# Performance work log

Hardware: AMD Instinct MI355X
Metric: run time of the kernel (lower is better)

The kernel has to match this reference:

```python
import jax, jax.numpy as jnp
import numpy as np

N, L, D = 4, 4096, 1024
H = 16
HD = D // H          # 64
MLP = 4 * D          # 4096
EPS = 1e-5

def log_g(x):
    # torch: where(x>=0, log(relu(x)+0.5), -softplus(-x))
    return jnp.where(x >= 0.0, jnp.log(jax.nn.relu(x) + 0.5), -jax.nn.softplus(-x))

def parallel_scan_log(log_coeffs, log_values):
    # log_coeffs: (B, L, C); log_values: (B, L+1, C)
    a_star = jnp.pad(jnp.cumsum(log_coeffs, axis=1), ((0, 0), (1, 0), (0, 0)))
    log_h = jax.lax.cumlogsumexp(log_values - a_star, axis=1)
    return jnp.exp(a_star[:, 1:] + log_h[:, 1:])

def layer_norm(x, gamma, beta):
    mu = jnp.mean(x, axis=-1, keepdims=True)
    var = jnp.var(x, axis=-1, keepdims=True)
    return (x - mu) * jax.lax.rsqrt(var + EPS) * gamma + beta

def setup_inputs() -> dict:
    key = jax.random.key(0)
    ks = jax.random.split(key, 12)
    s = 0.02
    return {
        "x": jax.random.normal(ks[0], (N, L, D), jnp.float32),
        "h_0": jax.random.normal(ks[1], (N, 1, D), jnp.float32),
        "w_in": jax.random.normal(ks[2], (D, D), jnp.float32) * s,
        "b_in": jnp.zeros((D,), jnp.float32),
        "wz": jax.random.normal(ks[3], (HD, HD), jnp.float32) * s,
        "bz": jnp.zeros((HD,), jnp.float32),
        "wh": jax.random.normal(ks[4], (HD, HD), jnp.float32) * s,
        "bh": jnp.zeros((HD,), jnp.float32),
        "w_out": jax.random.normal(ks[5], (D, D), jnp.float32) * s,
        "b_out": jnp.zeros((D,), jnp.float32),
        "ln1_g": jnp.ones((D,), jnp.float32),
        "ln1_b": jnp.zeros((D,), jnp.float32),
        "ln2_g": jnp.ones((D,), jnp.float32),
        "ln2_b": jnp.zeros((D,), jnp.float32),
        "mw1": jax.random.normal(ks[6], (D, MLP), jnp.float32) * s,
        "mb1": jnp.zeros((MLP,), jnp.float32),
        "mw2": jax.random.normal(ks[7], (MLP, MLP), jnp.float32) * s,
        "mb2": jnp.zeros((MLP,), jnp.float32),
        "mw3": jax.random.normal(ks[8], (MLP, D), jnp.float32) * s,
        "mb3": jnp.zeros((D,), jnp.float32),
    }

def reference(x, h_0, w_in, b_in, wz, bz, wh, bh, w_out, b_out,
              ln1_g, ln1_b, ln2_g, ln2_b, mw1, mb1, mw2, mb2, mw3, mb3):
    n, l, d = x.shape
    rnn_input = layer_norm(x, ln1_g, ln1_b)
    pi = rnn_input @ w_in + b_in                                 # (N,L,D)
    pi = pi.reshape(n, l, H, HD).transpose(0, 2, 1, 3).reshape(n * H, l, HD)
    h0 = h_0.reshape(n, 1, H, HD).transpose(0, 2, 1, 3).reshape(n * H, 1, HD)
    # minGRU in log-space
    k = pi @ wz + bz
    log_z = -jax.nn.softplus(-k)
    log_coeffs = -jax.nn.softplus(k)
    log_h0 = log_g(h0)
    log_th = log_g(pi @ wh + bh)
    h = parallel_scan_log(log_coeffs, jnp.concatenate([log_h0, log_z + log_th], axis=1))
    rnn_states = h.reshape(n, H, l, HD).transpose(0, 2, 1, 3).reshape(n, l, d)
    x = x + (rnn_states @ w_out + b_out)
    mlp_in = layer_norm(x, ln2_g, ln2_b)
    y = jax.nn.silu(mlp_in @ mw1 + mb1)
    y = jax.nn.silu(y @ mw2 + mb2)
    y = y @ mw3 + mb3
    return (x + y, rnn_states)
```

## Files before the change

kernel.cpp:

```cpp
#include <hip/hip_runtime.h>
#include <hip/hip_bf16.h>

typedef __attribute__((ext_vector_type(8))) short short8;
typedef __attribute__((ext_vector_type(4))) float f32x4;
using bf16 = __hip_bfloat16;

#define DEV static __device__ __forceinline__

DEV float bf2f(bf16 v) { return __bfloat162float(v); }
DEV bf16 f2bf(float v) { return __float2bfloat16(v); }

DEV void gld_lds16(const void* g, void* l) {
  __builtin_amdgcn_global_load_lds(
      (const __attribute__((address_space(1))) void*)g,
      (__attribute__((address_space(3))) void*)l, 16, 0, 0);
}

__global__ __launch_bounds__(256)
void wconv_kernel(const float* __restrict__ w, bf16* __restrict__ wT, int K, int N) {
  __shared__ float tile[32][33];
  const int kt = blockIdx.x * 32, nt = blockIdx.y * 32;
  const int tx = threadIdx.x & 31, ty = threadIdx.x >> 5;
#pragma unroll
  for (int i = 0; i < 32; i += 8)
    tile[ty + i][tx] = w[(size_t)(kt + ty + i) * N + nt + tx];
  __syncthreads();
#pragma unroll
  for (int i = 0; i < 32; i += 8)
    wT[(size_t)(nt + ty + i) * K + kt + tx] = f2bf(tile[tx][ty + i]);
}

__global__ __launch_bounds__(256)
void ln_kernel(const float* __restrict__ x, const float* __restrict__ g,
               const float* __restrict__ b, bf16* __restrict__ out) {
  const int row = blockIdx.x;
  const int t = threadIdx.x;
  const float4 v = ((const float4*)(x + (size_t)row * 1024))[t];
  float s = v.x + v.y + v.z + v.w;
  float ss = v.x * v.x + v.y * v.y + v.z * v.z + v.w * v.w;
#pragma unroll
  for (int off = 32; off > 0; off >>= 1) {
    s += __shfl_down(s, off);
    ss += __shfl_down(ss, off);
  }
  __shared__ float red[8];
  if ((t & 63) == 0) { red[(t >> 6) * 2] = s; red[(t >> 6) * 2 + 1] = ss; }
  __syncthreads();
  s = red[0] + red[2] + red[4] + red[6];
  ss = red[1] + red[3] + red[5] + red[7];
  const float mu = s * (1.f / 1024.f);
  const float rstd = rsqrtf(ss * (1.f / 1024.f) - mu * mu + 1e-5f);
  const float4 g4 = ((const float4*)g)[t];
  const float4 b4 = ((const float4*)b)[t];
  struct alignas(8) B4 { bf16 v[4]; } o;
  o.v[0] = f2bf((v.x - mu) * rstd * g4.x + b4.x);
  o.v[1] = f2bf((v.y - mu) * rstd * g4.y + b4.y);
  o.v[2] = f2bf((v.z - mu) * rstd * g4.z + b4.z);
  o.v[3] = f2bf((v.w - mu) * rstd * g4.w + b4.w);
  *(B4*)(out + (size_t)row * 1024 + t * 4) = o;
}

template <int EPI>
__global__ __launch_bounds__(256, 2)
void gemm128(const bf16* __restrict__ A, const bf16* __restrict__ BT,
             const float* __restrict__ bias, const float* __restrict__ res,
             void* __restrict__ C, int M, int N, int K) {
  __shared__ short As[128 * 64];
  __shared__ short Bs[128 * 64];
  const int tid = threadIdx.x;
  const int l = tid & 63;
  const int w = tid >> 6;
  const int wr = w >> 1, wc = w & 1;

  const int nbn = N >> 7;
  const int nwg = gridDim.x;
  const int bid = blockIdx.x;
  const int q = nwg >> 3, r = nwg & 7;
  const int xcd = bid & 7, lin = bid >> 3;
  const int wg = (xcd < r ? xcd * (q + 1) : r * (q + 1) + (xcd - r) * q) + lin;
  const int bm = wg / nbn, bn = wg % nbn;

  const bf16* Ab = A + (size_t)bm * 128 * K;
  const bf16* Bb = BT + (size_t)bn * 128 * K;

  f32x4 acc[4][4];
#pragma unroll
  for (int i = 0; i < 4; ++i)
#pragma unroll
    for (int j = 0; j < 4; ++j) acc[i][j] = (f32x4){0.f, 0.f, 0.f, 0.f};

  const int srow = l >> 3;
  const int scol = (((l & 7) ^ (l >> 3)) << 3);

  for (int k0 = 0; k0 < K; k0 += 64) {
    __syncthreads();
#pragma unroll
    for (int p = 0; p < 4; ++p) {
      const int rowA = p * 32 + w * 8 + srow;
      gld_lds16(Ab + (size_t)rowA * K + k0 + scol, As + (p * 32 + w * 8) * 64);
      gld_lds16(Bb + (size_t)rowA * K + k0 + scol, Bs + (p * 32 + w * 8) * 64);
    }
    __syncthreads();
    const int xr = (l & 7) << 3;
#pragma unroll
    for (int kk = 0; kk < 2; ++kk) {
      short8 fa[4], fb[4];
#pragma unroll
      for (int m = 0; m < 4; ++m)
        fa[m] = *(const short8*)&As[(wr * 64 + m * 16 + (l & 15)) * 64 +
                                    ((kk * 32 + (l >> 4) * 8) ^ xr)];
#pragma unroll
      for (int n = 0; n < 4; ++n)
        fb[n] = *(const short8*)&Bs[(wc * 64 + n * 16 + (l & 15)) * 64 +
                                    ((kk * 32 + (l >> 4) * 8) ^ xr)];
#pragma unroll
      for (int m = 0; m < 4; ++m)
#pragma unroll
        for (int n = 0; n < 4; ++n)
          acc[m][n] = __builtin_amdgcn_mfma_f32_16x16x32_bf16(fa[m], fb[n], acc[m][n], 0, 0, 0);
    }
  }

  const int lc = l & 15;
  const int lr = (l >> 4) * 4;
#pragma unroll
  for (int n = 0; n < 4; ++n) {
    const int col = bn * 128 + wc * 64 + n * 16 + lc;
    const float bv = bias[col];
#pragma unroll
    for (int m = 0; m < 4; ++m) {
      const int row = bm * 128 + wr * 64 + m * 16 + lr;
#pragma unroll
      for (int r2 = 0; r2 < 4; ++r2) {
        float v = acc[m][n][r2] + bv;
        const size_t off = (size_t)(row + r2) * N + col;
        if constexpr (EPI == 1) v = v / (1.f + __expf(-v));
        if constexpr (EPI == 2) {
          ((float*)C)[off] = res[off] + v;
        } else {
          ((bf16*)C)[off] = f2bf(v);
        }
      }
    }
  }
  (void)M;
}

template <int EPI>
__global__ __launch_bounds__(512, 2)
void gemm256(const bf16* __restrict__ A, const bf16* __restrict__ BT,
             const float* __restrict__ bias, const float* __restrict__ res,
             void* __restrict__ C, int M, int N, int K) {
  __shared__ alignas(16) short As[2][256 * 64];
  __shared__ alignas(16) short Bs[2][256 * 64];
  const int tid = threadIdx.x;
  const int l = tid & 63;
  const int w = tid >> 6;
  const int wr = w >> 2;
  const int wc = w & 3;

  const int nbn = N >> 8;
  const int nwg = gridDim.x;
  const int bid = blockIdx.x;
  const int q = nwg >> 3, r = nwg & 7;
  const int xcd = bid & 7, lin = bid >> 3;
  const int wg = (xcd < r ? xcd * (q + 1) : r * (q + 1) + (xcd - r) * q) + lin;
  const int bm = wg / nbn, bn = wg % nbn;

  const bf16* Ab = A + (size_t)bm * 256 * K;
  const bf16* Bb = BT + (size_t)bn * 256 * K;

  const int gcol = ((l & 7) ^ (l >> 3)) << 3;
  const int fr = l & 15;
  const int kq = (l >> 4) << 3;
  const int xr = (l & 7) << 3;

  f32x4 acc[8][4];
#pragma unroll
  for (int i = 0; i < 8; ++i)
#pragma unroll
    for (int j = 0; j < 4; ++j) acc[i][j] = (f32x4){0.f, 0.f, 0.f, 0.f};

  short8 fa[2][2], fb[4][2];

#define STAGE_A(BUF, HALF, KT)                                                     \
  do {                                                                             \
    const int rl_ = (HALF) * 128 + w * 16;                                         \
    gld_lds16(Ab + (size_t)(rl_ + (l >> 3)) * K + (KT) * 64 + gcol,                \
              &As[BUF][rl_ * 64]);                                                 \
    gld_lds16(Ab + (size_t)(rl_ + 8 + (l >> 3)) * K + (KT) * 64 + gcol,            \
              &As[BUF][(rl_ + 8) * 64]);                                           \
  } while (0)

#define STAGE_B(BUF, HALF, KT)                                                     \
  do {                                                                             \
    const int rl_ = (HALF) * 128 + w * 16;                                         \
    gld_lds16(Bb + (size_t)(rl_ + (l >> 3)) * K + (KT) * 64 + gcol,                \
              &Bs[BUF][rl_ * 64]);                                                 \
    gld_lds16(Bb + (size_t)(rl_ + 8 + (l >> 3)) * K + (KT) * 64 + gcol,            \
              &Bs[BUF][(rl_ + 8) * 64]);                                           \
  } while (0)

#define LDA2(BUF, M0)                                                                          \
  do {                                                                                         \
    fa[0][0] = *(const short8*)&As[BUF][(wr * 128 + (M0) * 16 + fr) * 64 + (kq ^ xr)];         \
    fa[0][1] = *(const short8*)&As[BUF][(wr * 128 + (M0) * 16 + fr) * 64 + ((32 + kq) ^ xr)];  \
    fa[1][0] = *(const short8*)&As[BUF][(wr * 128 + (M0)*16 + 16 + fr) * 64 + (kq ^ xr)];      \
    fa[1][1] = *(const short8*)&As[BUF][(wr * 128 + (M0)*16 + 16 + fr) * 64 + ((32 + kq) ^ xr)]; \
  } while (0)

#define LDB8(BUF)                                                                              \
  do {                                                                                         \
    _Pragma("unroll") for (int n_ = 0; n_ < 4; ++n_) {                                         \
      fb[n_][0] = *(const short8*)&Bs[BUF][(wc * 64 + n_ * 16 + fr) * 64 + (kq ^ xr)];         \
      fb[n_][1] = *(const short8*)&Bs[BUF][(wc * 64 + n_ * 16 + fr) * 64 + ((32 + kq) ^ xr)];  \
    }                                                                                          \
  } while (0)

#define MMA_PAIR(M0)                                                                           \
  do {                                                                                         \
    _Pragma("unroll") for (int n_ = 0; n_ < 4; ++n_) {                                         \
      acc[M0][n_] = __builtin_amdgcn_mfma_f32_16x16x32_bf16(fa[0][0], fb[n_][0], acc[M0][n_], 0, 0, 0); \
      acc[(M0) + 1][n_] = __builtin_amdgcn_mfma_f32_16x16x32_bf16(fa[1][0], fb[n_][0], acc[(M0) + 1][n_], 0, 0, 0); \
      acc[M0][n_] = __builtin_amdgcn_mfma_f32_16x16x32_bf16(fa[0][1], fb[n_][1], acc[M0][n_], 0, 0, 0); \
      acc[(M0) + 1][n_] = __builtin_amdgcn_mfma_f32_16x16x32_bf16(fa[1][1], fb[n_][1], acc[(M0) + 1][n_], 0, 0, 0); \
    }                                                                                          \
  } while (0)

#define PHASE(CBUF, M0, ...)                                                       \
  do {                                                                             \
    LDA2(CBUF, M0);                                                                \
    __VA_ARGS__;                                                                   \
    __builtin_amdgcn_s_barrier();                                                  \
    asm volatile("s_waitcnt lgkmcnt(0)");                                          \
    __builtin_amdgcn_s_setprio(1);                                                 \
    MMA_PAIR(M0);                                                                  \
    __builtin_amdgcn_s_setprio(0);                                                 \
    __builtin_amdgcn_s_barrier();                                                  \
  } while (0)

#define PHASE_END(CBUF, ...)                                                       \
  do {                                                                             \
    LDA2(CBUF, 6);                                                                 \
    __VA_ARGS__;                                                                   \
    __builtin_amdgcn_s_barrier();                                                  \
    asm volatile("s_waitcnt lgkmcnt(0)");                                          \
    __builtin_amdgcn_s_setprio(1);                                                 \
    MMA_PAIR(6);                                                                   \
    __builtin_amdgcn_s_setprio(0);                                                 \
    if (more) asm volatile("s_waitcnt vmcnt(4)" ::: "memory");                     \
    else      asm volatile("s_waitcnt vmcnt(0)" ::: "memory");                     \
    __builtin_amdgcn_s_barrier();                                                  \
  } while (0)

  STAGE_A(0, 0, 0); STAGE_A(0, 1, 0);
  STAGE_B(0, 0, 0); STAGE_B(0, 1, 0);
  STAGE_B(1, 0, 1); STAGE_B(1, 1, 1);
  asm volatile("s_waitcnt vmcnt(4)" ::: "memory");
  __builtin_amdgcn_s_barrier();

  const int NT = K >> 6;
  const int NI = NT >> 1;
#pragma unroll 1
  for (int i = 0; i < NI; ++i) {
    const int t0 = i * 2;
    const bool more = (i + 1) < NI;
    LDB8(0);
    PHASE(0, 0, STAGE_A(1, 0, t0 + 1));
    PHASE(0, 2, STAGE_A(1, 1, t0 + 1));
    PHASE(0, 4, if (more) STAGE_B(0, 0, t0 + 2));
    PHASE_END(0, if (more) STAGE_B(0, 1, t0 + 2));
    LDB8(1);
    PHASE(1, 0, if (more) STAGE_A(0, 0, t0 + 2));
    PHASE(1, 2, if (more) STAGE_A(0, 1, t0 + 2));
    PHASE(1, 4, if (more) STAGE_B(1, 0, t0 + 3));
    PHASE_END(1, if (more) STAGE_B(1, 1, t0 + 3));
  }

#undef STAGE_A
#undef STAGE_B
#undef LDA2
#undef LDB8
#undef MMA_PAIR
#undef PHASE
#undef PHASE_END

  const int lc = l & 15;
  const int lr = (l >> 4) * 4;
#pragma unroll
  for (int n = 0; n < 4; ++n) {
    const int col = bn * 256 + wc * 64 + n * 16 + lc;
    const float bv = bias[col];
#pragma unroll
    for (int m = 0; m < 8; ++m) {
      const int row = bm * 256 + wr * 128 + m * 16 + lr;
#pragma unroll
      for (int r2 = 0; r2 < 4; ++r2) {
        float v = acc[m][n][r2] + bv;
        const size_t off = (size_t)(row + r2) * N + col;
        if constexpr (EPI == 1) v = v / (1.f + __expf(-v));
        if constexpr (EPI == 2) {
          ((float*)C)[off] = res[off] + v;
        } else {
          ((bf16*)C)[off] = f2bf(v);
        }
      }
    }
  }
  (void)M;
}

__global__ __launch_bounds__(256)
void heads_kernel(const bf16* __restrict__ piB,
                  const float* __restrict__ wz, const float* __restrict__ bz,
                  const float* __restrict__ wh, const float* __restrict__ bh,
                  bf16* __restrict__ aB, bf16* __restrict__ bB) {
  __shared__ float wzs[4096], whs[4096], pis[4096];
  const int h = blockIdx.y;
  const int t0 = blockIdx.x * 64;
  const int tid = threadIdx.x;
#pragma unroll
  for (int i = tid; i < 4096; i += 256) {
    wzs[i] = wz[i];
    whs[i] = wh[i];
    pis[i] = bf2f(piB[(size_t)(t0 + (i >> 6)) * 1024 + h * 64 + (i & 63)]);
  }
  __syncthreads();
  const int hd = tid & 63;
  const int tb = (tid >> 6) * 16;
  float accK[16], accT[16];
  const float bzv = bz[hd], bhv = bh[hd];
#pragma unroll
  for (int i = 0; i < 16; ++i) { accK[i] = bzv; accT[i] = bhv; }
  for (int j = 0; j < 64; ++j) {
    const float wzv = wzs[j * 64 + hd];
    const float whv = whs[j * 64 + hd];
#pragma unroll
    for (int i = 0; i < 16; ++i) {
      const float p = pis[(tb + i) * 64 + j];
      accK[i] = fmaf(p, wzv, accK[i]);
      accT[i] = fmaf(p, whv, accT[i]);
    }
  }
#pragma unroll
  for (int i = 0; i < 16; ++i) {
    const float k = accK[i], th = accT[i];
    const float sig = 1.f / (1.f + __expf(-k));
    const float a = 1.f - sig;
    const float gg = th >= 0.f ? th + 0.5f : 1.f / (1.f + __expf(-th));
    const float bb = sig * gg;
    const size_t idx = (size_t)(t0 + tb + i) * 1024 + h * 64 + hd;
    aB[idx] = f2bf(a);
    bB[idx] = f2bf(bb);
  }
}

__global__ __launch_bounds__(256)
void scan_phase1(const bf16* __restrict__ aB, const bf16* __restrict__ bB,
                 float* __restrict__ cA, float* __restrict__ cB) {
  const int idx = blockIdx.x * 256 + threadIdx.x;
  const int c = idx & 1023;
  const int chunk = (idx >> 10) & 63;
  const int n = idx >> 16;
  size_t base = ((size_t)(n * 4096 + chunk * 64)) * 1024 + c;
  float A = 1.f, B = 0.f;
#pragma unroll 8
  for (int s = 0; s < 64; ++s) {
    const float a = bf2f(aB[base]);
    const float b = bf2f(bB[base]);
    A *= a;
    B = fmaf(a, B, b);
    base += 1024;
  }
  const size_t o = ((size_t)(n * 64 + chunk)) * 1024 + c;
  cA[o] = A;
  cB[o] = B;
}

__global__ __launch_bounds__(256)
void scan_phase2(const float* __restrict__ h0,
                 const float* __restrict__ cA, const float* __restrict__ cB,
                 float* __restrict__ hst) {
  const int idx = blockIdx.x * 256 + threadIdx.x;
  const int c = idx & 1023;
  const int n = idx >> 10;
  float hv = h0[(size_t)n * 1024 + c];
  hv = hv >= 0.f ? hv + 0.5f : 1.f / (1.f + __expf(-hv));
  for (int ch = 0; ch < 64; ++ch) {
    const size_t o = ((size_t)(n * 64 + ch)) * 1024 + c;
    hst[o] = hv;
    hv = fmaf(cA[o], hv, cB[o]);
  }
}

__global__ __launch_bounds__(256)
void scan_phase3(const bf16* __restrict__ aB, const bf16* __restrict__ bB,
                 const float* __restrict__ hst,
                 float* __restrict__ rnn, bf16* __restrict__ rnnB) {
  const int idx = blockIdx.x * 256 + threadIdx.x;
  const int c = idx & 1023;
  const int chunk = (idx >> 10) & 63;
  const int n = idx >> 16;
  float hv = hst[((size_t)(n * 64 + chunk)) * 1024 + c];
  size_t base = ((size_t)(n * 4096 + chunk * 64)) * 1024 + c;
#pragma unroll 4
  for (int s = 0; s < 64; ++s) {
    const float a = bf2f(aB[base]);
    const float b = bf2f(bB[base]);
    hv = fmaf(a, hv, b);
    rnn[base] = hv;
    rnnB[base] = f2bf(hv);
    base += 1024;
  }
}

extern "C" void kernel_launch(void* const* d_in, const int* in_sizes, int n_in,
                              void* d_out, int out_size, void* d_ws, size_t ws_size,
                              hipStream_t stream) {
  const float* x    = (const float*)d_in[0];
  const float* h0   = (const float*)d_in[1];
  const float* w_in = (const float*)d_in[2];
  const float* b_in = (const float*)d_in[3];
  const float* wz   = (const float*)d_in[4];
  const float* bz   = (const float*)d_in[5];
  const float* wh   = (const float*)d_in[6];
  const float* bh   = (const float*)d_in[7];
  const float* w_out= (const float*)d_in[8];
  const float* b_out= (const float*)d_in[9];
  const float* ln1g = (const float*)d_in[10];
  const float* ln1b = (const float*)d_in[11];
  const float* ln2g = (const float*)d_in[12];
  const float* ln2b = (const float*)d_in[13];
  const float* mw1  = (const float*)d_in[14];
  const float* mb1  = (const float*)d_in[15];
  const float* mw2  = (const float*)d_in[16];
  const float* mb2  = (const float*)d_in[17];
  const float* mw3  = (const float*)d_in[18];
  const float* mb3  = (const float*)d_in[19];
  (void)in_sizes; (void)n_in; (void)out_size;

  float* out0 = (float*)d_out;
  float* out1 = (float*)d_out + (size_t)16384 * 1024;

  char* ws = (char*)d_ws;
  size_t o = 0;
  auto take = [&](size_t bytes) { char* p = ws + o; o += (bytes + 255) & ~(size_t)255; return p; };
  bf16* w_inT = (bf16*)take((size_t)1024 * 1024 * 2);
  bf16* w_outT= (bf16*)take((size_t)1024 * 1024 * 2);
  bf16* mw1T  = (bf16*)take((size_t)4096 * 1024 * 2);
  bf16* mw2T  = (bf16*)take((size_t)4096 * 4096 * 2);
  bf16* mw3T  = (bf16*)take((size_t)4096 * 1024 * 2);
  bf16* lnxB  = (bf16*)take((size_t)16384 * 1024 * 2);
  bf16* piB   = (bf16*)take((size_t)16384 * 1024 * 2);
  bf16* aB    = (bf16*)take((size_t)16384 * 1024 * 2);
  bf16* bB    = (bf16*)take((size_t)16384 * 1024 * 2);
  float* cA   = (float*)take((size_t)4 * 64 * 1024 * 4);
  float* cB   = (float*)take((size_t)4 * 64 * 1024 * 4);
  float* hst  = (float*)take((size_t)4 * 64 * 1024 * 4);
  if (o > ws_size) return;

  wconv_kernel<<<dim3(32, 32), 256, 0, stream>>>(w_in, w_inT, 1024, 1024);
  wconv_kernel<<<dim3(32, 32), 256, 0, stream>>>(w_out, w_outT, 1024, 1024);
  wconv_kernel<<<dim3(32, 128), 256, 0, stream>>>(mw1, mw1T, 1024, 4096);
  wconv_kernel<<<dim3(128, 128), 256, 0, stream>>>(mw2, mw2T, 4096, 4096);
  wconv_kernel<<<dim3(128, 32), 256, 0, stream>>>(mw3, mw3T, 4096, 1024);

  ln_kernel<<<16384, 256, 0, stream>>>(x, ln1g, ln1b, lnxB);
  gemm256<0><<<256, 512, 0, stream>>>(lnxB, w_inT, b_in, nullptr, piB, 16384, 1024, 1024);

  heads_kernel<<<dim3(256, 16), 256, 0, stream>>>(piB, wz, bz, wh, bh, aB, bB);
  scan_phase1<<<1024, 256, 0, stream>>>(aB, bB, cA, cB);
  scan_phase2<<<16, 256, 0, stream>>>(h0, cA, cB, hst);
  scan_phase3<<<1024, 256, 0, stream>>>(aB, bB, hst, out1, lnxB );

  gemm256<2><<<256, 512, 0, stream>>>(lnxB, w_outT, b_out, x, out0, 16384, 1024, 1024);

  ln_kernel<<<16384, 256, 0, stream>>>(out0, ln2g, ln2b, lnxB );
  bf16* t1 = aB;
  bf16* t2 = bB;
  for (int mc = 0; mc < 4; ++mc) {
    const bf16* a3 = lnxB + (size_t)mc * 4096 * 1024;
    gemm256<1><<<256, 512, 0, stream>>>(a3, mw1T, mb1, nullptr, t1, 4096, 4096, 1024);
    gemm256<1><<<256, 512, 0, stream>>>(t1, mw2T, mb2, nullptr, t2, 4096, 4096, 4096);
    float* oc = out0 + (size_t)mc * 4096 * 1024;
    gemm128<2><<<256, 256, 0, stream>>>(t2, mw3T, mb3, oc, oc, 4096, 1024, 4096);
  }
}
```

Before: 1.352 ms.

## Double-buffer MFMA register fragments to overlap LDS reads with matrix math

```diff
diff --git a/kernel.cpp b/kernel.cpp
--- a/kernel.cpp
+++ b/kernel.cpp
@@ -175,115 +175,145 @@
   const int kq = (l >> 4) << 3;
   const int xr = (l & 7) << 3;
 
+  const bf16* Abl = Ab + (size_t)(w * 16 + (l >> 3)) * K + gcol;
+  const bf16* Bbl = Bb + (size_t)(w * 16 + (l >> 3)) * K + gcol;
+
   f32x4 acc[8][4];
 #pragma unroll
   for (int i = 0; i < 8; ++i)
 #pragma unroll
     for (int j = 0; j < 4; ++j) acc[i][j] = (f32x4){0.f, 0.f, 0.f, 0.f};
 
-  short8 fa[2][2], fb[4][2];
+  short8 fa[2][2][2];
+  short8 fb[2][4][2];
+
+#define BARX() __builtin_amdgcn_s_barrier()
 
 #define STAGE_A(BUF, HALF, KT)                                                     \
   do {                                                                             \
-    const int rl_ = (HALF) * 128 + w * 16;                                         \
-    gld_lds16(Ab + (size_t)(rl_ + (l >> 3)) * K + (KT) * 64 + gcol,                \
-              &As[BUF][rl_ * 64]);                                                 \
-    gld_lds16(Ab + (size_t)(rl_ + 8 + (l >> 3)) * K + (KT) * 64 + gcol,            \
-              &As[BUF][(rl_ + 8) * 64]);                                           \
+    gld_lds16(Abl + (size_t)((HALF) * 128) * K + (size_t)(KT) * 64,                \
+              &As[BUF][((HALF) * 128 + w * 16) * 64]);                             \
+    gld_lds16(Abl + (size_t)((HALF) * 128 + 8) * K + (size_t)(KT) * 64,            \
+              &As[BUF][((HALF) * 128 + w * 16 + 8) * 64]);                         \
   } while (0)
 
 #define STAGE_B(BUF, HALF, KT)                                                     \
   do {                                                                             \
-    const int rl_ = (HALF) * 128 + w * 16;                                         \
-    gld_lds16(Bb + (size_t)(rl_ + (l >> 3)) * K + (KT) * 64 + gcol,                \
-              &Bs[BUF][rl_ * 64]);                                                 \
-    gld_lds16(Bb + (size_t)(rl_ + 8 + (l >> 3)) * K + (KT) * 64 + gcol,            \
-              &Bs[BUF][(rl_ + 8) * 64]);                                           \
+    gld_lds16(Bbl + (size_t)((HALF) * 128) * K + (size_t)(KT) * 64,                \
+              &Bs[BUF][((HALF) * 128 + w * 16) * 64]);                             \
+    gld_lds16(Bbl + (size_t)((HALF) * 128 + 8) * K + (size_t)(KT) * 64,            \
+              &Bs[BUF][((HALF) * 128 + w * 16 + 8) * 64]);                         \
   } while (0)
 
-#define LDA2(BUF, M0)                                                                          \
-  do {                                                                                         \
-    fa[0][0] = *(const short8*)&As[BUF][(wr * 128 + (M0) * 16 + fr) * 64 + (kq ^ xr)];         \
-    fa[0][1] = *(const short8*)&As[BUF][(wr * 128 + (M0) * 16 + fr) * 64 + ((32 + kq) ^ xr)];  \
-    fa[1][0] = *(const short8*)&As[BUF][(wr * 128 + (M0)*16 + 16 + fr) * 64 + (kq ^ xr)];      \
-    fa[1][1] = *(const short8*)&As[BUF][(wr * 128 + (M0)*16 + 16 + fr) * 64 + ((32 + kq) ^ xr)]; \
+#define RD_FA(S, BUF, Q)                                                                         \
+  do {                                                                                           \
+    fa[S][0][0] = *(const short8*)&As[BUF][(wr * 128 + (Q)*32 + fr) * 64 + (kq ^ xr)];           \
+    fa[S][0][1] = *(const short8*)&As[BUF][(wr * 128 + (Q)*32 + fr) * 64 + ((32 + kq) ^ xr)];    \
+    fa[S][1][0] = *(const short8*)&As[BUF][(wr * 128 + (Q)*32 + 16 + fr) * 64 + (kq ^ xr)];      \
+    fa[S][1][1] = *(const short8*)&As[BUF][(wr * 128 + (Q)*32 + 16 + fr) * 64 + ((32 + kq) ^ xr)]; \
   } while (0)
 
-#define LDB8(BUF)                                                                              \
-  do {                                                                                         \
-    _Pragma("unroll") for (int n_ = 0; n_ < 4; ++n_) {                                         \
-      fb[n_][0] = *(const short8*)&Bs[BUF][(wc * 64 + n_ * 16 + fr) * 64 + (kq ^ xr)];         \
-      fb[n_][1] = *(const short8*)&Bs[BUF][(wc * 64 + n_ * 16 + fr) * 64 + ((32 + kq) ^ xr)];  \
-    }                                                                                          \
+#define RD_FB_H(S, BUF, H)                                                                       \
+  do {                                                                                           \
+    _Pragma("unroll") for (int n_ = 0; n_ < 4; ++n_)                                             \
+        fb[S][n_][H] =                                                                           \
+        *(const short8*)&Bs[BUF][(wc * 64 + n_ * 16 + fr) * 64 + (((H)*32 + kq) ^ xr)];          \
   } while (0)
 
-#define MMA_PAIR(M0)                                                                           \
-  do {                                                                                         \
-    _Pragma("unroll") for (int n_ = 0; n_ < 4; ++n_) {                                         \
-      acc[M0][n_] = __builtin_amdgcn_mfma_f32_16x16x32_bf16(fa[0][0], fb[n_][0], acc[M0][n_], 0, 0, 0); \
-      acc[(M0) + 1][n_] = __builtin_amdgcn_mfma_f32_16x16x32_bf16(fa[1][0], fb[n_][0], acc[(M0) + 1][n_], 0, 0, 0); \
-      acc[M0][n_] = __builtin_amdgcn_mfma_f32_16x16x32_bf16(fa[0][1], fb[n_][1], acc[M0][n_], 0, 0, 0); \
-      acc[(M0) + 1][n_] = __builtin_amdgcn_mfma_f32_16x16x32_bf16(fa[1][1], fb[n_][1], acc[(M0) + 1][n_], 0, 0, 0); \
-    }                                                                                          \
-  } while (0)
-
-#define PHASE(CBUF, M0, ...)                                                       \
-  do {                                                                             \
-    LDA2(CBUF, M0);                                                                \
-    __VA_ARGS__;                                                                   \
-    __builtin_amdgcn_s_barrier();                                                  \
-    asm volatile("s_waitcnt lgkmcnt(0)");                                          \
-    __builtin_amdgcn_s_setprio(1);                                                 \
-    MMA_PAIR(M0);                                                                  \
-    __builtin_amdgcn_s_setprio(0);                                                 \
-    __builtin_amdgcn_s_barrier();                                                  \
-  } while (0)
-
-#define PHASE_END(CBUF, ...)                                                       \
-  do {                                                                             \
-    LDA2(CBUF, 6);                                                                 \
-    __VA_ARGS__;                                                                   \
-    __builtin_amdgcn_s_barrier();                                                  \
-    asm volatile("s_waitcnt lgkmcnt(0)");                                          \
-    __builtin_amdgcn_s_setprio(1);                                                 \
-    MMA_PAIR(6);                                                                   \
-    __builtin_amdgcn_s_setprio(0);                                                 \
-    if (more) asm volatile("s_waitcnt vmcnt(4)" ::: "memory");                     \
-    else      asm volatile("s_waitcnt vmcnt(0)" ::: "memory");                     \
-    __builtin_amdgcn_s_barrier();                                                  \
+#define MMA_Q(FAS, FBS, Q)                                                                       \
+  do {                                                                                           \
+    __builtin_amdgcn_s_setprio(1);                                                               \
+    _Pragma("unroll") for (int n_ = 0; n_ < 4; ++n_) {                                           \
+      acc[2 * (Q)][n_] = __builtin_amdgcn_mfma_f32_16x16x32_bf16(fa[FAS][0][0], fb[FBS][n_][0],  \
+                                                                 acc[2 * (Q)][n_], 0, 0, 0);     \
+      acc[2 * (Q) + 1][n_] = __builtin_amdgcn_mfma_f32_16x16x32_bf16(                            \
+          fa[FAS][1][0], fb[FBS][n_][0], acc[2 * (Q) + 1][n_], 0, 0, 0);                         \
+    }                                                                                            \
+    _Pragma("unroll") for (int n_ = 0; n_ < 4; ++n_) {                                           \
+      acc[2 * (Q)][n_] = __builtin_amdgcn_mfma_f32_16x16x32_bf16(fa[FAS][0][1], fb[FBS][n_][1],  \
+                                                                 acc[2 * (Q)][n_], 0, 0, 0);     \
+      acc[2 * (Q) + 1][n_] = __builtin_amdgcn_mfma_f32_16x16x32_bf16(                            \
+          fa[FAS][1][1], fb[FBS][n_][1], acc[2 * (Q) + 1][n_], 0, 0, 0);                         \
+    }                                                                                            \
+    __builtin_amdgcn_s_setprio(0);                                                               \
   } while (0)
 
   STAGE_A(0, 0, 0); STAGE_A(0, 1, 0);
   STAGE_B(0, 0, 0); STAGE_B(0, 1, 0);
   STAGE_B(1, 0, 1); STAGE_B(1, 1, 1);
   asm volatile("s_waitcnt vmcnt(4)" ::: "memory");
-  __builtin_amdgcn_s_barrier();
+  BARX();
+  RD_FB_H(0, 0, 0);
+  RD_FB_H(0, 0, 1);
+  RD_FA(0, 0, 0);
 
   const int NT = K >> 6;
   const int NI = NT >> 1;
 #pragma unroll 1
   for (int i = 0; i < NI; ++i) {
-    const int t0 = i * 2;
+    const int t0 = 2 * i;
     const bool more = (i + 1) < NI;
-    LDB8(0);
-    PHASE(0, 0, STAGE_A(1, 0, t0 + 1));
-    PHASE(0, 2, STAGE_A(1, 1, t0 + 1));
-    PHASE(0, 4, if (more) STAGE_B(0, 0, t0 + 2));
-    PHASE_END(0, if (more) STAGE_B(0, 1, t0 + 2));
-    LDB8(1);
-    PHASE(1, 0, if (more) STAGE_A(0, 0, t0 + 2));
-    PHASE(1, 2, if (more) STAGE_A(0, 1, t0 + 2));
-    PHASE(1, 4, if (more) STAGE_B(1, 0, t0 + 3));
-    PHASE_END(1, if (more) STAGE_B(1, 1, t0 + 3));
-  }
-
+    RD_FA(1, 0, 1);
+    STAGE_A(1, 0, t0 + 1);
+    BARX();
+    MMA_Q(0, 0, 0);
+    BARX();
+    RD_FA(0, 0, 2);
+    STAGE_A(1, 1, t0 + 1);
+    BARX();
+    MMA_Q(1, 0, 1);
+    BARX();
+    asm volatile("s_waitcnt vmcnt(4)" ::: "memory");
+    RD_FA(1, 0, 3);
+    RD_FB_H(1, 1, 0);
+    if (more) STAGE_B(0, 0, t0 + 2);
+    BARX();
+    MMA_Q(0, 0, 2);
+    BARX();
+    if (more) asm volatile("s_waitcnt vmcnt(2)" ::: "memory");
+    else      asm volatile("s_waitcnt vmcnt(0)" ::: "memory");
+    RD_FA(0, 1, 0);
+    RD_FB_H(1, 1, 1);
+    if (more) STAGE_B(0, 1, t0 + 2);
+    BARX();
+    MMA_Q(1, 0, 3);
+    BARX();
+    RD_FA(1, 1, 1);
+    if (more) STAGE_A(0, 0, t0 + 2);
+    BARX();
+    MMA_Q(0, 1, 0);
+    BARX();
+    RD_FA(0, 1, 2);
+    if (more) STAGE_A(0, 1, t0 + 2);
+    BARX();
+    MMA_Q(1, 1, 1);
+    BARX();
+    asm volatile("s_waitcnt vmcnt(4)" ::: "memory");
+    RD_FA(1, 1, 3);
+    if (more) {
+      RD_FB_H(0, 0, 0);
+      STAGE_B(1, 0, t0 + 3);
+    }
+    BARX();
+    MMA_Q(0, 1, 2);
+    BARX();
+    if (more) {
+      asm volatile("s_waitcnt vmcnt(2)" ::: "memory");
+      RD_FA(0, 0, 0);
+      RD_FB_H(0, 0, 1);
+      STAGE_B(1, 1, t0 + 3);
+    }
+    BARX();
+    MMA_Q(1, 1, 3);
+    BARX();
+  }
+
+#undef BARX
 #undef STAGE_A
 #undef STAGE_B
-#undef LDA2
-#undef LDB8
-#undef MMA_PAIR
-#undef PHASE
-#undef PHASE_END
+#undef RD_FA
+#undef RD_FB_H
+#undef MMA_Q
 
   const int lc = l & 15;
   const int lr = (l >> 4) * 4;
```

New measurement: 1.991 ms. +47.3%, slower.
